# Kernel optimization log

Measured on AMD Instinct MI355X. Metric: run time of the kernel, lower is better.

## Reference

```python
import jax, jax.numpy as jnp
import numpy as np

B, T, D_IN, H, D_OUT = 64, 512, 256, 512, 128


def setup_inputs() -> dict:
    key = jax.random.key(0)
    ks = jax.random.split(key, 12)
    s = 1.0 / np.sqrt(H)  # PyTorch RNN/Linear init scale
    u = lambda k, shp, sc: jax.random.uniform(k, shp, jnp.float32, -sc, sc)
    return {
        "x": jax.random.normal(ks[0], (B, T, D_IN), jnp.float32),
        "w_ih0": u(ks[1], (H, D_IN), s),
        "w_hh0": u(ks[2], (H, H), s),
        "b_ih0": u(ks[3], (H,), s),
        "b_hh0": u(ks[4], (H,), s),
        "w_ih1": u(ks[5], (H, H), s),
        "w_hh1": u(ks[6], (H, H), s),
        "b_ih1": u(ks[7], (H,), s),
        "b_hh1": u(ks[8], (H,), s),
        "w_fc": u(ks[9], (D_OUT, H), s),
        "b_fc": u(ks[10], (D_OUT,), s),
    }


def _rnn_layer(xs, w_ih, w_hh, b_ih, b_hh):
    """One vanilla tanh RNN layer. xs: (B, T, D) -> (outputs (B, T, H), last hidden (B, H)).
    h_t = tanh(x_t @ W_ih^T + b_ih + h_{t-1} @ W_hh^T + b_hh)
    """
    # Precompute the input projection for all timesteps at once (one big GEMM).
    xproj = jnp.einsum("btd,hd->bth", xs, w_ih) + b_ih + b_hh  # (B, T, H)

    def step(h, xp_t):
        h_new = jnp.tanh(xp_t + h @ w_hh.T)
        return h_new, h_new

    h0 = jnp.zeros((xs.shape[0], w_hh.shape[0]), xs.dtype)
    h_last, hs = jax.lax.scan(step, h0, jnp.swapaxes(xproj, 0, 1))  # scan over T
    return jnp.swapaxes(hs, 0, 1), h_last


def reference(x, w_ih0, w_hh0, b_ih0, b_hh0, w_ih1, w_hh1, b_ih1, b_hh1, w_fc, b_fc):
    h1_seq, _ = _rnn_layer(x, w_ih0, w_hh0, b_ih0, b_hh0)      # layer 0: full sequence
    _, h_last = _rnn_layer(h1_seq, w_ih1, w_hh1, b_ih1, b_hh1)  # layer 1: only final state needed
    # last_time_step_out = rnn_out[:, -1, :] == h_last of the top layer
    return h_last @ w_fc.T + b_fc  # (B, D_OUT)
```

## Files before the change

### kernel.cpp

```cpp
#include <hip/hip_runtime.h>

#define B_    64
#define T_    512
#define DIN_  256
#define H_    512
#define DOUT_ 128

#define CHUNK  32
#define NCHUNK (T_ / CHUNK)
#define NGEMM  64

typedef _Float16 f16x8 __attribute__((ext_vector_type(8)));
typedef float    f32x4 __attribute__((ext_vector_type(4)));
typedef _Float16 half2v __attribute__((ext_vector_type(2)));

__device__ __forceinline__ float dot8(uint4 w, uint4 h, float s) {
#if __has_builtin(__builtin_amdgcn_fdot2)
  s = __builtin_amdgcn_fdot2(__builtin_bit_cast(half2v, w.x), __builtin_bit_cast(half2v, h.x), s, false);
  s = __builtin_amdgcn_fdot2(__builtin_bit_cast(half2v, w.y), __builtin_bit_cast(half2v, h.y), s, false);
  s = __builtin_amdgcn_fdot2(__builtin_bit_cast(half2v, w.z), __builtin_bit_cast(half2v, h.z), s, false);
  s = __builtin_amdgcn_fdot2(__builtin_bit_cast(half2v, w.w), __builtin_bit_cast(half2v, h.w), s, false);
#else
  const half2v* wp = (const half2v*)&w;
  const half2v* hp = (const half2v*)&h;
#pragma unroll
  for (int q = 0; q < 4; ++q) {
    s += (float)wp[q][0] * (float)hp[q][0] + (float)wp[q][1] * (float)hp[q][1];
  }
#endif
  return s;
}

__device__ __forceinline__ float fast_tanh(float x) {
  float a = fabsf(x);
  float e = __expf(2.f * a);
  float r = 1.f - 2.f / (e + 1.f);
  return copysignf(r, x);
}

__device__ __forceinline__ void pin4(uint4& v) {
  asm volatile("" : "+v"(v.x), "+v"(v.y), "+v"(v.z), "+v"(v.w));
}

__device__ __forceinline__ unsigned ld_flag(const unsigned* p) {
  return __hip_atomic_load(p, __ATOMIC_RELAXED, __HIP_MEMORY_SCOPE_AGENT);
}
__device__ __forceinline__ void add_flag(unsigned* p) {
  __hip_atomic_fetch_add(p, 1u, __ATOMIC_RELEASE, __HIP_MEMORY_SCOPE_AGENT);
}
__device__ __forceinline__ void wait_flag(const unsigned* p, unsigned target) {
  for (int n = 0; n < (1 << 21); ++n) {
    if (ld_flag(p) >= target) return;
    __builtin_amdgcn_s_sleep(8);
  }
}

__global__ void cvt_f32_f16(const float* __restrict__ in, _Float16* __restrict__ out, int n) {
  int idx = blockIdx.x * 256 + threadIdx.x;
  if (idx < n) out[idx] = (_Float16)in[idx];
}

__global__ void zero_flags(unsigned* __restrict__ f) {
  if (threadIdx.x < 2 * NCHUNK) f[threadIdx.x] = 0u;
}

__global__ void prep_w(const float* __restrict__ w0, const float* __restrict__ w1,
                       _Float16* __restrict__ o0, _Float16* __restrict__ o1) {
  int idx = blockIdx.x * 256 + threadIdx.x;
  const float* src = (idx < 32768) ? w0 : w1;
  _Float16* dst = (idx < 32768) ? o0 : o1;
  int c = idx & 32767;
  int tid  = c & 511;
  int rest = c >> 9;
  int i    = rest & 15;
  int rsub = rest >> 4;
  int row = 4 * (tid & 127) + rsub;
  int kc  = (tid >> 7) * 16 + i;
#pragma unroll
  for (int e = 0; e < 8; ++e)
    dst[(size_t)c * 8 + e] = (_Float16)src[row * 512 + kc * 8 + e];
}

__global__ __launch_bounds__(256)
void gemm_xproj(const _Float16* __restrict__ X,
                const _Float16* __restrict__ W,
                const float* __restrict__ bias1,
                const float* __restrict__ bias2,
                _Float16* __restrict__ out, int K) {
  __shared__ __align__(16) _Float16 As[128 * 32];
  __shared__ __align__(16) _Float16 Bs[128 * 32];
  const int tid  = threadIdx.x;
  const int wave = tid >> 6;
  const int lane = tid & 63;
  const int wr = wave >> 1, wc = wave & 1;
  const int m0 = blockIdx.x * 128, n0 = blockIdx.y * 128;
  const int fr = lane & 15;
  const int fk = (lane >> 4) * 8;
  const int cA = (lane & 3) * 8;
  const int rsub = lane >> 2;

  f32x4 acc[4][4];
#pragma unroll
  for (int a = 0; a < 4; ++a)
#pragma unroll
    for (int b = 0; b < 4; ++b)
      acc[a][b] = (f32x4){0.f, 0.f, 0.f, 0.f};

  for (int k0 = 0; k0 < K; k0 += 32) {
    __syncthreads();
#pragma unroll
    for (int q = 0; q < 2; ++q) {
      int p = wave * 2 + q;
      int r = p * 16 + rsub;
      const _Float16* gA = X + (size_t)(m0 + r) * K + (k0 + cA);
      const _Float16* gB = W + (size_t)(n0 + r) * K + (k0 + cA);
      __builtin_amdgcn_global_load_lds(
          (const __attribute__((address_space(1))) void*)gA,
          (__attribute__((address_space(3))) void*)((char*)As + p * 1024), 16, 0, 0);
      __builtin_amdgcn_global_load_lds(
          (const __attribute__((address_space(1))) void*)gB,
          (__attribute__((address_space(3))) void*)((char*)Bs + p * 1024), 16, 0, 0);
    }
    __syncthreads();

    f16x8 af[4], bfr[4];
#pragma unroll
    for (int mt = 0; mt < 4; ++mt)
      af[mt] = *(const f16x8*)&As[(wr * 64 + mt * 16 + fr) * 32 + fk];
#pragma unroll
    for (int nt = 0; nt < 4; ++nt)
      bfr[nt] = *(const f16x8*)&Bs[(wc * 64 + nt * 16 + fr) * 32 + fk];
#pragma unroll
    for (int mt = 0; mt < 4; ++mt)
#pragma unroll
      for (int nt = 0; nt < 4; ++nt)
        acc[mt][nt] = __builtin_amdgcn_mfma_f32_16x16x32_f16(af[mt], bfr[nt], acc[mt][nt], 0, 0, 0);
  }

  const int col = lane & 15, rq = lane >> 4;
#pragma unroll
  for (int nt = 0; nt < 4; ++nt) {
    int n = n0 + wc * 64 + nt * 16 + col;
    float bias = bias1[n] + bias2[n];
#pragma unroll
    for (int mt = 0; mt < 4; ++mt) {
      int mbase = m0 + wr * 64 + mt * 16 + rq * 4;
#pragma unroll
      for (int r = 0; r < 4; ++r)
        out[(size_t)(mbase + r) * H_ + n] = (_Float16)(acc[mt][nt][r] + bias);
    }
  }
}

__device__ __forceinline__ void scan_role(
    int layer, int b,
    const uint4* __restrict__ Wg, const _Float16* __restrict__ xproj,
    _Float16* __restrict__ seq, float* __restrict__ hlast,
    unsigned* __restrict__ ca, unsigned* __restrict__ cb, char* smem)
{
  uint4* ldsW = (uint4*)smem;
  _Float16 (*hb)[512] = (_Float16 (*)[512])(smem + 49152);
  float (*psum)[512] = (float (*)[512])(smem + 51200);
  const int tid = threadIdx.x;
  const int u = tid >> 7;

  uint4 wreg[32];
#pragma unroll
  for (int i = 0; i < 32; ++i) wreg[i] = Wg[i * 512 + tid];
#pragma unroll
  for (int i = 0; i < 32; ++i) pin4(wreg[i]);

#pragma unroll
  for (int i = 0; i < 6; ++i) ldsW[i * 512 + tid] = Wg[(32 + i) * 512 + tid];

  hb[0][tid] = (_Float16)0.f;
  hb[1][tid] = (_Float16)0.f;
  __syncthreads();

  const uint4* S2 = Wg + (size_t)38 * 512 + tid;
  const uint4* S3 = Wg + (size_t)48 * 512 + tid;
  const _Float16* xp = xproj + (size_t)b * (T_ * H_) + tid;
  _Float16* sq = seq + (size_t)b * (T_ * H_) + tid;

  int cur = 0;
  for (int t = 0; t < T_; ++t) {
    if (layer == 1 && (t & (CHUNK - 1)) == 0) {
      if (tid == 0) wait_flag(cb + (t / CHUNK), NGEMM);
      __syncthreads();
      __threadfence();
    }
    float xv = (float)xp[(size_t)t * H_];
    const uint4* hbu = (const uint4*)hb[cur] + u * 16;

    uint4 q2[4], q3[4];
#pragma unroll
    for (int p = 0; p < 4; ++p) {
      q2[p] = S2[(size_t)p * 512];
      q3[p] = S3[(size_t)p * 512];
    }

    float a0 = 0.f, a1 = 0.f, a2 = 0.f, a3 = 0.f;
#pragma unroll
    for (int i = 0; i < 16; ++i) {
      uint4 h = hbu[i];
      a0 = dot8(wreg[i], h, a0);
      a1 = dot8(wreg[16 + i], h, a1);
      if (i < 6) {
        a2 = dot8(ldsW[i * 512 + tid], h, a2);
      } else {
        a2 = dot8(q2[(i - 6) & 3], h, a2);
        if (i - 6 + 4 < 10) q2[(i - 6) & 3] = S2[(size_t)(i - 2) * 512];
      }
      a3 = dot8(q3[i & 3], h, a3);
      if (i + 4 < 16) q3[i & 3] = S3[(size_t)(i + 4) * 512];
    }
    *(f32x4*)&psum[u][4 * (tid & 127)] = (f32x4){a0, a1, a2, a3};
    __syncthreads();

    float s = (psum[0][tid] + psum[1][tid]) + (psum[2][tid] + psum[3][tid]);
    float hn = fast_tanh(s + xv);
    _Float16 h16 = (_Float16)hn;
    hb[cur ^ 1][tid] = h16;
    if (layer == 0) {
      sq[(size_t)t * H_] = h16;
    } else if (t == T_ - 1) {
      hlast[b * H_ + tid] = hn;
    }
    __syncthreads();
    cur ^= 1;
    if (layer == 0 && (t & (CHUNK - 1)) == CHUNK - 1) {
      if (tid == 0) { __threadfence(); add_flag(ca + (t / CHUNK)); }
    }
  }
}

__device__ __forceinline__ void gemm_role(
    int g,
    const _Float16* __restrict__ X,
    const _Float16* __restrict__ W,
    const float* __restrict__ bias1, const float* __restrict__ bias2,
    _Float16* __restrict__ out,
    unsigned* __restrict__ ca, unsigned* __restrict__ cb, char* smem)
{
  _Float16* As = (_Float16*)smem;
  _Float16* Bs = (_Float16*)(smem + 8192);
  const int tid  = threadIdx.x;
  const int wave = tid >> 6;
  const int lane = tid & 63;
  const int wr = wave >> 1, wc = wave & 1;
  const int mt = g >> 2;
  const int n0 = (g & 3) * 128;
  const int fr = lane & 15;
  const int fk = (lane >> 4) * 8;
  const int sr  = tid >> 2;
  const int scq = (tid & 3) * 8;
  const int col = lane & 15, rq = lane >> 4;
  const size_t wrow = (size_t)(n0 + sr) * H_ + scq;

  for (int c = 0; c < NCHUNK; ++c) {
    if (tid == 0) wait_flag(ca + c, B_);
    __syncthreads();
    __threadfence();

    const size_t arow =
        ((size_t)(4 * mt + (sr >> 5)) * T_ + c * CHUNK + (sr & 31)) * H_ + scq;

    f32x4 acc[2][4];
#pragma unroll
    for (int m = 0; m < 2; ++m)
#pragma unroll
      for (int n = 0; n < 4; ++n)
        acc[m][n] = (f32x4){0.f, 0.f, 0.f, 0.f};

    for (int k0 = 0; k0 < H_; k0 += 32) {
      __syncthreads();
      __builtin_amdgcn_global_load_lds(
          (const __attribute__((address_space(1))) void*)(X + arow + k0),
          (__attribute__((address_space(3))) void*)((char*)As + (tid >> 6) * 1024), 16, 0, 0);
      __builtin_amdgcn_global_load_lds(
          (const __attribute__((address_space(1))) void*)(W + wrow + k0),
          (__attribute__((address_space(3))) void*)((char*)Bs + (tid >> 6) * 1024), 16, 0, 0);
      __syncthreads();

      f16x8 af[2], bf[4];
#pragma unroll
      for (int m = 0; m < 2; ++m)
        af[m] = *(const f16x8*)&As[(wr * 32 + m * 16 + fr) * 32 + fk];
#pragma unroll
      for (int n = 0; n < 4; ++n)
        bf[n] = *(const f16x8*)&Bs[(wc * 64 + n * 16 + fr) * 32 + fk];
#pragma unroll
      for (int m = 0; m < 2; ++m)
#pragma unroll
        for (int n = 0; n < 4; ++n)
          acc[m][n] = __builtin_amdgcn_mfma_f32_16x16x32_f16(af[m], bf[n], acc[m][n], 0, 0, 0);
    }

#pragma unroll
    for (int n = 0; n < 4; ++n) {
      int nn = n0 + wc * 64 + n * 16 + col;
      float bias = bias1[nn] + bias2[nn];
#pragma unroll
      for (int m = 0; m < 2; ++m) {
        int jbase = wr * 32 + m * 16 + rq * 4;
#pragma unroll
        for (int r = 0; r < 4; ++r) {
          int jj = jbase + r;
          size_t row = ((size_t)(4 * mt + (jj >> 5)) * T_ + c * CHUNK + (jj & 31)) * (size_t)H_;
          out[row + nn] = (_Float16)(acc[m][n][r] + bias);
        }
      }
    }
    __syncthreads();
    if (tid == 0) { __threadfence(); add_flag(cb + c); }
  }
}

__global__ __launch_bounds__(512, 1)
void fused_pipeline(const uint4* __restrict__ Wg0, const uint4* __restrict__ Wg1,
                    const _Float16* __restrict__ Wih1,
                    const float* __restrict__ b_ih1, const float* __restrict__ b_hh1,
                    _Float16* __restrict__ xproj, _Float16* __restrict__ h1seq,
                    float* __restrict__ hlast, unsigned* __restrict__ flags) {
  __shared__ __align__(16) char smem[59392];
  unsigned* ca = flags;
  unsigned* cb = flags + NCHUNK;
  const int wg = blockIdx.x;
  if (wg < 64) {
    scan_role(0, wg, Wg0, xproj, h1seq, hlast, ca, cb, smem);
  } else if (wg < 128) {
    scan_role(1, wg - 64, Wg1, xproj, h1seq, hlast, ca, cb, smem);
  } else {
    gemm_role(wg - 128, h1seq, Wih1, b_ih1, b_hh1, xproj, ca, cb, smem);
  }
}

__global__ void fc_kernel(const float* __restrict__ h2,
                          const float* __restrict__ wfc,
                          const float* __restrict__ bfc,
                          float* __restrict__ out) {
  int b = blockIdx.x, o = threadIdx.x;
  float s = bfc[o];
  const float* hv = h2 + b * H_;
  const float* wr = wfc + (size_t)o * H_;
#pragma unroll 8
  for (int k = 0; k < H_; ++k) s += hv[k] * wr[k];
  out[b * DOUT_ + o] = s;
}

extern "C" void kernel_launch(void* const* d_in, const int* in_sizes, int n_in,
                              void* d_out, int out_size, void* d_ws, size_t ws_size,
                              hipStream_t stream) {
  const float* x     = (const float*)d_in[0];
  const float* w_ih0 = (const float*)d_in[1];
  const float* w_hh0 = (const float*)d_in[2];
  const float* b_ih0 = (const float*)d_in[3];
  const float* b_hh0 = (const float*)d_in[4];
  const float* w_ih1 = (const float*)d_in[5];
  const float* w_hh1 = (const float*)d_in[6];
  const float* b_ih1 = (const float*)d_in[7];
  const float* b_hh1 = (const float*)d_in[8];
  const float* w_fc  = (const float*)d_in[9];
  const float* b_fc  = (const float*)d_in[10];

  char* ws = (char*)d_ws;
  _Float16* Ws0   = (_Float16*)(ws + 0);
  _Float16* Ws1   = (_Float16*)(ws + 524288);
  _Float16* Wih0  = (_Float16*)(ws + 1048576);
  _Float16* Wih1  = (_Float16*)(ws + 1310720);
  float*    h2    = (float*)   (ws + 2097152);
  unsigned* flags = (unsigned*)(ws + 3145728);
  _Float16* xproj = (_Float16*)(ws + 4194304);
  _Float16* xf16  = (_Float16*)(ws + 37748736);
  _Float16* h1seq = (_Float16*)(ws + 37748736);

  cvt_f32_f16<<<32768, 256, 0, stream>>>(x, xf16, B_ * T_ * DIN_);
  cvt_f32_f16<<<512,   256, 0, stream>>>(w_ih0, Wih0, H_ * DIN_);
  cvt_f32_f16<<<1024,  256, 0, stream>>>(w_ih1, Wih1, H_ * H_);
  prep_w<<<256, 256, 0, stream>>>(w_hh0, w_hh1, Ws0, Ws1);
  zero_flags<<<1, 64, 0, stream>>>(flags);

  gemm_xproj<<<dim3(256, 4), 256, 0, stream>>>(xf16, Wih0, b_ih0, b_hh0, xproj, DIN_);

  fused_pipeline<<<192, 512, 0, stream>>>((const uint4*)Ws0, (const uint4*)Ws1,
                                          Wih1, b_ih1, b_hh1,
                                          xproj, h1seq, h2, flags);

  fc_kernel<<<B_, DOUT_, 0, stream>>>(h2, w_fc, b_fc, (float*)d_out);
}
```

Measured before the change: 1.221 ms.

## Re-partition recurrent matvec to 8-way K split with more register-resident weights

```diff
diff --git a/kernel.cpp b/kernel.cpp
--- a/kernel.cpp
+++ b/kernel.cpp
@@ -42,6 +42,11 @@
   asm volatile("" : "+v"(v.x), "+v"(v.y), "+v"(v.z), "+v"(v.w));
 }
 
+__device__ __forceinline__ void barrier_lds() {
+  asm volatile("s_waitcnt lgkmcnt(0)" ::: "memory");
+  __builtin_amdgcn_s_barrier();
+}
+
 __device__ __forceinline__ unsigned ld_flag(const unsigned* p) {
   return __hip_atomic_load(p, __ATOMIC_RELAXED, __HIP_MEMORY_SCOPE_AGENT);
 }
@@ -71,11 +76,11 @@
   _Float16* dst = (idx < 32768) ? o0 : o1;
   int c = idx & 32767;
   int tid  = c & 511;
-  int rest = c >> 9;
-  int i    = rest & 15;
-  int rsub = rest >> 4;
-  int row = 4 * (tid & 127) + rsub;
-  int kc  = (tid >> 7) * 16 + i;
+  int slot = c >> 9;
+  int i = slot & 7;
+  int s = slot >> 3;
+  int row = 8 * (tid & 63) + s;
+  int kc  = (tid >> 6) * 8 + i;
 #pragma unroll
   for (int e = 0; e < 8; ++e)
     dst[(size_t)c * 8 + e] = (_Float16)src[row * 512 + kc * 8 + e];
@@ -158,29 +163,35 @@
     _Float16* __restrict__ seq, float* __restrict__ hlast,
     unsigned* __restrict__ ca, unsigned* __restrict__ cb, char* smem)
 {
-  uint4* ldsW = (uint4*)smem;
-  _Float16 (*hb)[512] = (_Float16 (*)[512])(smem + 49152);
-  float (*psum)[512] = (float (*)[512])(smem + 51200);
+  float* psumA = (float*)smem;
+  float* psumB = (float*)(smem + 8192);
+  _Float16 (*hb)[512] = (_Float16 (*)[512])(smem + 16384);
   const int tid = threadIdx.x;
-  const int u = tid >> 7;
-
-  uint4 wreg[32];
-#pragma unroll
-  for (int i = 0; i < 32; ++i) wreg[i] = Wg[i * 512 + tid];
-#pragma unroll
-  for (int i = 0; i < 32; ++i) pin4(wreg[i]);
-
-#pragma unroll
-  for (int i = 0; i < 6; ++i) ldsW[i * 512 + tid] = Wg[(32 + i) * 512 + tid];
+  const int u = tid >> 6;
+  const int r = tid & 63;
+
+  uint4 wreg[40];
+#pragma unroll
+  for (int i = 0; i < 40; ++i) wreg[i] = Wg[i * 512 + tid];
+#pragma unroll
+  for (int i = 0; i < 40; ++i) pin4(wreg[i]);
 
   hb[0][tid] = (_Float16)0.f;
   hb[1][tid] = (_Float16)0.f;
   __syncthreads();
 
-  const uint4* S2 = Wg + (size_t)38 * 512 + tid;
-  const uint4* S3 = Wg + (size_t)48 * 512 + tid;
+  const uint4* S5 = Wg + (size_t)40 * 512 + tid;
+  const uint4* S6 = Wg + (size_t)48 * 512 + tid;
+  const uint4* S7 = Wg + (size_t)56 * 512 + tid;
   const _Float16* xp = xproj + (size_t)b * (T_ * H_) + tid;
   _Float16* sq = seq + (size_t)b * (T_ * H_) + tid;
+
+  uint4 q5[2], q6[2], q7[2];
+  q5[0] = S5[0];            q5[1] = S5[512];
+  q6[0] = S6[0];            q6[1] = S6[512];
+  q7[0] = S7[0];            q7[1] = S7[512];
+
+  const float* pred = ((tid & 4) ? psumB : psumA) + 4 * (tid >> 3) + (tid & 3);
 
   int cur = 0;
   for (int t = 0; t < T_; ++t) {
@@ -190,34 +201,31 @@
       __threadfence();
     }
     float xv = (float)xp[(size_t)t * H_];
-    const uint4* hbu = (const uint4*)hb[cur] + u * 16;
-
-    uint4 q2[4], q3[4];
-#pragma unroll
-    for (int p = 0; p < 4; ++p) {
-      q2[p] = S2[(size_t)p * 512];
-      q3[p] = S3[(size_t)p * 512];
-    }
+    const uint4* hbu = (const uint4*)hb[cur] + u * 8;
 
     float a0 = 0.f, a1 = 0.f, a2 = 0.f, a3 = 0.f;
-#pragma unroll
-    for (int i = 0; i < 16; ++i) {
+    float a4 = 0.f, a5 = 0.f, a6 = 0.f, a7 = 0.f;
+#pragma unroll
+    for (int i = 0; i < 8; ++i) {
       uint4 h = hbu[i];
-      a0 = dot8(wreg[i], h, a0);
-      a1 = dot8(wreg[16 + i], h, a1);
-      if (i < 6) {
-        a2 = dot8(ldsW[i * 512 + tid], h, a2);
-      } else {
-        a2 = dot8(q2[(i - 6) & 3], h, a2);
-        if (i - 6 + 4 < 10) q2[(i - 6) & 3] = S2[(size_t)(i - 2) * 512];
-      }
-      a3 = dot8(q3[i & 3], h, a3);
-      if (i + 4 < 16) q3[i & 3] = S3[(size_t)(i + 4) * 512];
-    }
-    *(f32x4*)&psum[u][4 * (tid & 127)] = (f32x4){a0, a1, a2, a3};
-    __syncthreads();
-
-    float s = (psum[0][tid] + psum[1][tid]) + (psum[2][tid] + psum[3][tid]);
+      a0 = dot8(wreg[i],      h, a0);
+      a1 = dot8(wreg[8 + i],  h, a1);
+      a2 = dot8(wreg[16 + i], h, a2);
+      a3 = dot8(wreg[24 + i], h, a3);
+      a4 = dot8(wreg[32 + i], h, a4);
+      a5 = dot8(q5[i & 1], h, a5);
+      q5[i & 1] = S5[(size_t)((i + 2) & 7) * 512];
+      a6 = dot8(q6[i & 1], h, a6);
+      q6[i & 1] = S6[(size_t)((i + 2) & 7) * 512];
+      a7 = dot8(q7[i & 1], h, a7);
+      q7[i & 1] = S7[(size_t)((i + 2) & 7) * 512];
+    }
+    *(f32x4*)&psumA[u * 256 + 4 * r] = (f32x4){a0, a1, a2, a3};
+    *(f32x4*)&psumB[u * 256 + 4 * r] = (f32x4){a4, a5, a6, a7};
+    barrier_lds();
+
+    float s = (((pred[0] + pred[256]) + (pred[512] + pred[768])) +
+               ((pred[1024] + pred[1280]) + (pred[1536] + pred[1792])));
     float hn = fast_tanh(s + xv);
     _Float16 h16 = (_Float16)hn;
     hb[cur ^ 1][tid] = h16;
@@ -226,11 +234,13 @@
     } else if (t == T_ - 1) {
       hlast[b * H_ + tid] = hn;
     }
-    __syncthreads();
+    if (layer == 0 && (t & (CHUNK - 1)) == CHUNK - 1) {
+      __syncthreads();
+      if (tid == 0) { __threadfence(); add_flag(ca + (t / CHUNK)); }
+    } else {
+      barrier_lds();
+    }
     cur ^= 1;
-    if (layer == 0 && (t & (CHUNK - 1)) == CHUNK - 1) {
-      if (tid == 0) { __threadfence(); add_flag(ca + (t / CHUNK)); }
-    }
   }
 }
 
@@ -322,7 +332,7 @@
                     const float* __restrict__ b_ih1, const float* __restrict__ b_hh1,
                     _Float16* __restrict__ xproj, _Float16* __restrict__ h1seq,
                     float* __restrict__ hlast, unsigned* __restrict__ flags) {
-  __shared__ __align__(16) char smem[59392];
+  __shared__ __align__(16) char smem[18432];
   unsigned* ca = flags;
   unsigned* cb = flags + NCHUNK;
   const int wg = blockIdx.x;
```

Result: slower. 2.916 ms (+138.7%).
